# Kernel tuning notes

Hardware: AMD Instinct MI355X
Metric: run time of the kernel (lower is better)

The kernel has to match this reference:

```python
import jax, jax.numpy as jnp
import numpy as np


def _kabsch_rmsd(p, c):
    # p, c: [N, 3]
    pm = jnp.mean(p, axis=0)  # [3]
    cm = jnp.mean(c, axis=0)  # [3]
    # 3x3 cross-covariance
    A = (p - pm).T @ (c - cm)
    U, S, Vt = jnp.linalg.svd(A, full_matrices=False)
    d = jnp.sign(jnp.linalg.det(A))
    # corr_mat = diag([1, 1, d]);  rotation = U @ corr_mat @ Vt
    scale = jnp.concatenate([jnp.ones((2,), dtype=p.dtype), d[None].astype(p.dtype)])
    R = U @ (scale[:, None] * Vt)  # [3,3]
    # translation = pm - R @ cm; aligned coords = (R @ c^T)^T + translation
    aligned = c @ R.T + (pm - R @ cm)
    sq = jnp.sum((p - aligned) ** 2, axis=1)  # [N]
    return jnp.sqrt(jnp.mean(sq))


def setup_inputs() -> dict:
    key = jax.random.key(0)
    k1, k2 = jax.random.split(key)
    B, N = 4096, 2048
    coords_pred = jax.random.normal(k1, (B, N, 3), dtype=jnp.float32)
    coords = jax.random.normal(k2, (B, N, 3), dtype=jnp.float32)
    return {"coords_pred": coords_pred, "coords": coords}


def reference(coords_pred, coords):
    # Batched Kabsch alignment + RMSD; default mode='global', return_all=False
    # -> mean over the per-sample RMSDs.
    rmsds = jax.vmap(_kabsch_rmsd)(coords_pred, coords)  # [B]
    return jnp.mean(rmsds)
```

## Files before the change

kernel.cpp:

```cpp
#include <hip/hip_runtime.h>
#include <math.h>

#define NPTS 2048
#define NF4 (NPTS * 3 / 4)
#define BLOCK 256
#define CHUNKS (NF4 / BLOCK)
#define PPT (NPTS / BLOCK)

__global__ __launch_bounds__(BLOCK, 3) void kabsch_kernel(
    const float* __restrict__ P, const float* __restrict__ C,
    float* __restrict__ rmsd_out, int B) {
  __shared__ float4 sP[NF4];
  __shared__ float4 sC[NF4];
  __shared__ float red[BLOCK / 64][17];

  const int b = blockIdx.x;
  const int t = threadIdx.x;
  const float4* p4 = (const float4*)(P + (size_t)b * (NPTS * 3));
  const float4* c4 = (const float4*)(C + (size_t)b * (NPTS * 3));

#pragma unroll
  for (int c = 0; c < CHUNKS; c++) {
    const int idx = c * BLOCK + t;
    __builtin_amdgcn_global_load_lds(
        (const __attribute__((address_space(1))) void*)(p4 + idx),
        (__attribute__((address_space(3))) void*)(&sP[idx]), 16, 0, 0);
    __builtin_amdgcn_global_load_lds(
        (const __attribute__((address_space(1))) void*)(c4 + idx),
        (__attribute__((address_space(3))) void*)(&sC[idx]), 16, 0, 0);
  }
  __syncthreads();

  const float* Pf = (const float*)sP;
  const float* Cf = (const float*)sC;

  float acc[17];
#pragma unroll
  for (int i = 0; i < 17; i++) acc[i] = 0.f;

#pragma unroll
  for (int k = 0; k < PPT; k++) {
    const int pt = k * BLOCK + t;
    const float px = Pf[3 * pt], py = Pf[3 * pt + 1], pz = Pf[3 * pt + 2];
    const float cx = Cf[3 * pt], cy = Cf[3 * pt + 1], cz = Cf[3 * pt + 2];
    acc[0] += px; acc[1] += py; acc[2] += pz;
    acc[3] += cx; acc[4] += cy; acc[5] += cz;
    acc[6] += px * px + py * py + pz * pz;
    acc[7] += cx * cx + cy * cy + cz * cz;
    acc[8]  += px * cx; acc[9]  += px * cy; acc[10] += px * cz;
    acc[11] += py * cx; acc[12] += py * cy; acc[13] += py * cz;
    acc[14] += pz * cx; acc[15] += pz * cy; acc[16] += pz * cz;
  }

#pragma unroll
  for (int off = 32; off > 0; off >>= 1) {
#pragma unroll
    for (int i = 0; i < 17; i++) acc[i] += __shfl_down(acc[i], off);
  }
  const int wave = t >> 6, lane = t & 63;
  if (lane == 0) {
#pragma unroll
    for (int i = 0; i < 17; i++) red[wave][i] = acc[i];
  }
  __syncthreads();

  if (t == 0) {
    float s[17];
#pragma unroll
    for (int i = 0; i < 17; i++)
      s[i] = red[0][i] + red[1][i] + red[2][i] + red[3][i];
    const float invN = 1.0f / (float)NPTS;
    const float spx = s[0], spy = s[1], spz = s[2];
    const float scx = s[3], scy = s[4], scz = s[5];
    const float Ep = s[6] - (spx * spx + spy * spy + spz * spz) * invN;
    const float Ec = s[7] - (scx * scx + scy * scy + scz * scz) * invN;
    const float a00 = s[8]  - spx * scx * invN, a01 = s[9]  - spx * scy * invN, a02 = s[10] - spx * scz * invN;
    const float a10 = s[11] - spy * scx * invN, a11 = s[12] - spy * scy * invN, a12 = s[13] - spy * scz * invN;
    const float a20 = s[14] - spz * scx * invN, a21 = s[15] - spz * scy * invN, a22 = s[16] - spz * scz * invN;
    const float det = a00 * (a11 * a22 - a12 * a21)
                    - a01 * (a10 * a22 - a12 * a20)
                    + a02 * (a10 * a21 - a11 * a20);
    const float b00 = a00 * a00 + a10 * a10 + a20 * a20;
    const float b11 = a01 * a01 + a11 * a11 + a21 * a21;
    const float b22 = a02 * a02 + a12 * a12 + a22 * a22;
    const float b01 = a00 * a01 + a10 * a11 + a20 * a21;
    const float b02 = a00 * a02 + a10 * a12 + a20 * a22;
    const float b12 = a01 * a02 + a11 * a12 + a21 * a22;
    const float q = (b00 + b11 + b22) * (1.f / 3.f);
    const float p1 = b01 * b01 + b02 * b02 + b12 * b12;
    const float d0 = b00 - q, d1 = b11 - q, d2 = b22 - q;
    const float p2 = d0 * d0 + d1 * d1 + d2 * d2 + 2.f * p1;
    float e1, e2, e3;
    if (p2 < 1e-20f) {
      e1 = e2 = e3 = q;
    } else {
      const float pp = sqrtf(p2 * (1.f / 6.f));
      const float inv = 1.f / pp;
      const float c00 = d0 * inv, c11 = d1 * inv, c22 = d2 * inv;
      const float c01 = b01 * inv, c02 = b02 * inv, c12 = b12 * inv;
      float r = 0.5f * (c00 * (c11 * c22 - c12 * c12)
                      - c01 * (c01 * c22 - c12 * c02)
                      + c02 * (c01 * c12 - c11 * c02));
      r = fminf(1.f, fmaxf(-1.f, r));
      const float phi = acosf(r) * (1.f / 3.f);
      e1 = q + 2.f * pp * cosf(phi);
      e3 = q + 2.f * pp * cosf(phi + 2.0943951023931953f);
      e2 = 3.f * q - e1 - e3;
    }
    const float s1 = sqrtf(fmaxf(e1, 0.f));
    const float s2 = sqrtf(fmaxf(e2, 0.f));
    const float s3 = sqrtf(fmaxf(e3, 0.f));
    const float dsign = (det > 0.f) ? 1.f : ((det < 0.f) ? -1.f : 0.f);
    const float trRS = s1 + s2 + dsign * s3;
    const float msd = (Ep + Ec - 2.f * trRS) * invN;
    rmsd_out[b] = sqrtf(fmaxf(msd, 0.f));
  }
}

__global__ __launch_bounds__(BLOCK) void mean_kernel(
    const float* __restrict__ rmsd, float* __restrict__ out, int B) {
  float s = 0.f;
  for (int i = threadIdx.x; i < B; i += BLOCK) s += rmsd[i];
#pragma unroll
  for (int off = 32; off > 0; off >>= 1) s += __shfl_down(s, off);
  __shared__ float sm[BLOCK / 64];
  const int wave = threadIdx.x >> 6, lane = threadIdx.x & 63;
  if (lane == 0) sm[wave] = s;
  __syncthreads();
  if (threadIdx.x == 0) {
    float tot = 0.f;
    for (int w = 0; w < BLOCK / 64; w++) tot += sm[w];
    out[0] = tot / (float)B;
  }
}

extern "C" void kernel_launch(void* const* d_in, const int* in_sizes, int n_in,
                              void* d_out, int out_size, void* d_ws, size_t ws_size,
                              hipStream_t stream) {
  const float* P = (const float*)d_in[0];
  const float* C = (const float*)d_in[1];
  float* out = (float*)d_out;
  float* ws = (float*)d_ws;
  const int B = in_sizes[0] / (NPTS * 3);
  kabsch_kernel<<<B, BLOCK, 0, stream>>>(P, C, ws, B);
  mean_kernel<<<1, BLOCK, 0, stream>>>(ws, out, B);
}
```

Measured before the change: 219.2 us.

## Load coordinates directly into registers with nontemporal vector loads, drop LDS staging

```diff
diff --git a/kernel.cpp b/kernel.cpp
--- a/kernel.cpp
+++ b/kernel.cpp
@@ -2,47 +2,41 @@
 #include <math.h>
 
 #define NPTS 2048
-#define NF4 (NPTS * 3 / 4)
-#define BLOCK 256
-#define CHUNKS (NF4 / BLOCK)
-#define PPT (NPTS / BLOCK)
+#define BLOCK 512
+#define NWAVE (BLOCK / 64)
 
-__global__ __launch_bounds__(BLOCK, 3) void kabsch_kernel(
+typedef float vfloat4 __attribute__((ext_vector_type(4)));
+
+__global__ __launch_bounds__(BLOCK, 4) void kabsch_kernel(
     const float* __restrict__ P, const float* __restrict__ C,
     float* __restrict__ rmsd_out, int B) {
-  __shared__ float4 sP[NF4];
-  __shared__ float4 sC[NF4];
-  __shared__ float red[BLOCK / 64][17];
-
   const int b = blockIdx.x;
   const int t = threadIdx.x;
-  const float4* p4 = (const float4*)(P + (size_t)b * (NPTS * 3));
-  const float4* c4 = (const float4*)(C + (size_t)b * (NPTS * 3));
+  const vfloat4* p4 = (const vfloat4*)(P + (size_t)b * (NPTS * 3));
+  const vfloat4* c4 = (const vfloat4*)(C + (size_t)b * (NPTS * 3));
 
-#pragma unroll
-  for (int c = 0; c < CHUNKS; c++) {
-    const int idx = c * BLOCK + t;
-    __builtin_amdgcn_global_load_lds(
-        (const __attribute__((address_space(1))) void*)(p4 + idx),
-        (__attribute__((address_space(3))) void*)(&sP[idx]), 16, 0, 0);
-    __builtin_amdgcn_global_load_lds(
-        (const __attribute__((address_space(1))) void*)(c4 + idx),
-        (__attribute__((address_space(3))) void*)(&sC[idx]), 16, 0, 0);
-  }
-  __syncthreads();
-
-  const float* Pf = (const float*)sP;
-  const float* Cf = (const float*)sC;
+  const int base = 3 * t;
+  const vfloat4 pa = __builtin_nontemporal_load(&p4[base]);
+  const vfloat4 pb = __builtin_nontemporal_load(&p4[base + 1]);
+  const vfloat4 pq = __builtin_nontemporal_load(&p4[base + 2]);
+  const vfloat4 ca = __builtin_nontemporal_load(&c4[base]);
+  const vfloat4 cb = __builtin_nontemporal_load(&c4[base + 1]);
+  const vfloat4 cq = __builtin_nontemporal_load(&c4[base + 2]);
 
   float acc[17];
 #pragma unroll
   for (int i = 0; i < 17; i++) acc[i] = 0.f;
 
+  const float Px[4] = {pa.x, pa.w, pb.z, pq.y};
+  const float Py[4] = {pa.y, pb.x, pb.w, pq.z};
+  const float Pz[4] = {pa.z, pb.y, pq.x, pq.w};
+  const float Cx[4] = {ca.x, ca.w, cb.z, cq.y};
+  const float Cy[4] = {ca.y, cb.x, cb.w, cq.z};
+  const float Cz[4] = {ca.z, cb.y, cq.x, cq.w};
 #pragma unroll
-  for (int k = 0; k < PPT; k++) {
-    const int pt = k * BLOCK + t;
-    const float px = Pf[3 * pt], py = Pf[3 * pt + 1], pz = Pf[3 * pt + 2];
-    const float cx = Cf[3 * pt], cy = Cf[3 * pt + 1], cz = Cf[3 * pt + 2];
+  for (int i = 0; i < 4; i++) {
+    const float px = Px[i], py = Py[i], pz = Pz[i];
+    const float cx = Cx[i], cy = Cy[i], cz = Cz[i];
     acc[0] += px; acc[1] += py; acc[2] += pz;
     acc[3] += cx; acc[4] += cy; acc[5] += cz;
     acc[6] += px * px + py * py + pz * pz;
@@ -57,6 +51,7 @@
 #pragma unroll
     for (int i = 0; i < 17; i++) acc[i] += __shfl_down(acc[i], off);
   }
+  __shared__ float red[NWAVE][17];
   const int wave = t >> 6, lane = t & 63;
   if (lane == 0) {
 #pragma unroll
@@ -67,8 +62,12 @@
   if (t == 0) {
     float s[17];
 #pragma unroll
-    for (int i = 0; i < 17; i++)
-      s[i] = red[0][i] + red[1][i] + red[2][i] + red[3][i];
+    for (int i = 0; i < 17; i++) {
+      float v = red[0][i];
+#pragma unroll
+      for (int w = 1; w < NWAVE; w++) v += red[w][i];
+      s[i] = v;
+    }
     const float invN = 1.0f / (float)NPTS;
     const float spx = s[0], spy = s[1], spz = s[2];
     const float scx = s[3], scy = s[4], scz = s[5];
@@ -117,19 +116,19 @@
   }
 }
 
-__global__ __launch_bounds__(BLOCK) void mean_kernel(
+__global__ __launch_bounds__(256) void mean_kernel(
     const float* __restrict__ rmsd, float* __restrict__ out, int B) {
   float s = 0.f;
-  for (int i = threadIdx.x; i < B; i += BLOCK) s += rmsd[i];
+  for (int i = threadIdx.x; i < B; i += 256) s += rmsd[i];
 #pragma unroll
   for (int off = 32; off > 0; off >>= 1) s += __shfl_down(s, off);
-  __shared__ float sm[BLOCK / 64];
+  __shared__ float sm[4];
   const int wave = threadIdx.x >> 6, lane = threadIdx.x & 63;
   if (lane == 0) sm[wave] = s;
   __syncthreads();
   if (threadIdx.x == 0) {
     float tot = 0.f;
-    for (int w = 0; w < BLOCK / 64; w++) tot += sm[w];
+    for (int w = 0; w < 4; w++) tot += sm[w];
     out[0] = tot / (float)B;
   }
 }
@@ -143,5 +142,5 @@
   float* ws = (float*)d_ws;
   const int B = in_sizes[0] / (NPTS * 3);
   kabsch_kernel<<<B, BLOCK, 0, stream>>>(P, C, ws, B);
-  mean_kernel<<<1, BLOCK, 0, stream>>>(ws, out, B);
+  mean_kernel<<<1, 256, 0, stream>>>(ws, out, B);
 }
```

New measurement: 221.5 us. Within noise of the previous version (+1.1%).
